# Performance work log

Measured on AMD Instinct MI355X. Metric: run time of the kernel, lower is better.

## Reference

```python
import jax, jax.numpy as jnp
import numpy as np

N, B, T, D = 4, 4, 512, 512
H, DK, DV = 8, 64, 64
LN_EPS = 1e-5


def setup_inputs() -> dict:
    key = jax.random.key(0)
    ks = jax.random.split(key, 5)
    s = 1.0 / np.sqrt(D)
    return {
        "x": jax.random.normal(ks[0], (N, B, T, D), jnp.float32),
        "Wq": jax.random.normal(ks[1], (D, H * DK), jnp.float32) * s,
        "bq": jnp.zeros((H * DK,), jnp.float32),
        "Wk": jax.random.normal(ks[2], (D, H * DK), jnp.float32) * s,
        "bk": jnp.zeros((H * DK,), jnp.float32),
        "Wv": jax.random.normal(ks[3], (D, H * DV), jnp.float32) * s,
        "bv": jnp.zeros((H * DV,), jnp.float32),
        "Wo": jax.random.normal(ks[4], (H * DV, D), jnp.float32) * (1.0 / np.sqrt(H * DV)),
        "bo": jnp.zeros((D,), jnp.float32),
        "gamma": jnp.ones((D,), jnp.float32),
        "beta": jnp.zeros((D,), jnp.float32),
    }


def reference(x, Wq, bq, Wk, bk, Wv, bv, Wo, bo, gamma, beta):
    # x: [N, B, T, D] -- N variables, each [B, T, D]
    n = x.shape[0]
    # Project once per variable (the torch code redundantly recomputes K/V per query var).
    q = (x @ Wq + bq).reshape(n, B, T, H, DK).transpose(0, 1, 3, 2, 4)  # [N,B,H,T,DK]
    k = (x @ Wk + bk).reshape(n, B, T, H, DK).transpose(0, 1, 3, 2, 4)  # [N,B,H,T,DK]
    v = (x @ Wv + bv).reshape(n, B, T, H, DV).transpose(0, 1, 3, 2, 4)  # [N,B,H,T,DV]
    # All-pairs attention: softmax over keys of EACH key-variable separately.
    scores = jnp.einsum('qbhtk,cbhsk->qcbhts', q, k) / np.sqrt(DK)  # [Nq,Nc,B,H,T,T]
    attn = jax.nn.softmax(scores, axis=-1)
    ctx = jnp.einsum('qcbhts,cbhsv->qcbhtv', attn, v)  # [Nq,Nc,B,H,T,DV]
    ctx = ctx.transpose(0, 1, 2, 4, 3, 5).reshape(n, n, B, T, H * DV)
    out = ctx @ Wo + bo                     # per-pair output projection
    out = out.sum(axis=1) / n               # average over key variables -> [N,B,T,D]
    res = x + out
    mu = res.mean(axis=-1, keepdims=True)
    var = res.var(axis=-1, keepdims=True)
    y = (res - mu) / jnp.sqrt(var + LN_EPS) * gamma + beta
    return y
```

## Files before the change

### kernel.cpp

```cpp
#include <hip/hip_runtime.h>


typedef __bf16 bf16x8 __attribute__((ext_vector_type(8)));
typedef __bf16 bf16x4 __attribute__((ext_vector_type(4)));
typedef short shortx4 __attribute__((ext_vector_type(4)));
typedef float floatx4 __attribute__((ext_vector_type(4)));
typedef float floatx16 __attribute__((ext_vector_type(16)));
typedef unsigned short ushortx8 __attribute__((ext_vector_type(8)));

static __device__ __forceinline__ unsigned short f2bf(float f) {
  union { __bf16 h; unsigned short u; } c; c.h = (__bf16)f; return c.u;
}
static __device__ __forceinline__ float bf2f(unsigned short u) {
  union { unsigned u32; float f; } c; c.u32 = ((unsigned)u) << 16; return c.f;
}

#define QSCALE 0.18033688011112042f
#define SHIFT2 (-17.312340489609306f)

__global__ __launch_bounds__(256) void prep(
    const float* __restrict__ Wq, const float* __restrict__ Wk,
    const float* __restrict__ Wv, const float* __restrict__ Wo,
    const float* __restrict__ x,
    unsigned short* __restrict__ wqkvT, unsigned short* __restrict__ woT,
    unsigned short* __restrict__ x_bf)
{
  const int bid = blockIdx.x;
  const int tid = threadIdx.x;
  if (bid < 256) {
    __shared__ unsigned short lds[64][65];
    const int z = bid >> 6, rest = bid & 63;
    const int k0 = (rest >> 3) * 64, n0 = (rest & 7) * 64;
    const float* W; unsigned short* T;
    if (z == 0)      { W = Wq; T = wqkvT; }
    else if (z == 1) { W = Wk; T = wqkvT + 262144; }
    else if (z == 2) { W = Wv; T = wqkvT + 524288; }
    else             { W = Wo; T = woT; }
    const int xx = tid & 63, yy = tid >> 6;
#pragma unroll
    for (int i = 0; i < 16; ++i) {
      const int row = yy * 16 + i;
      lds[row][xx] = f2bf(W[(size_t)(k0 + row) * 512 + n0 + xx]);
    }
    __syncthreads();
#pragma unroll
    for (int i = 0; i < 16; ++i) {
      const int nr = yy * 16 + i;
      T[(size_t)(n0 + nr) * 512 + k0 + xx] = lds[xx][nr];
    }
  } else {
    const int i = (bid - 256) * 256 + tid;
    const float4 a = ((const float4*)x)[i * 2];
    const float4 b = ((const float4*)x)[i * 2 + 1];
    ushortx8 o;
    o[0] = f2bf(a.x); o[1] = f2bf(a.y); o[2] = f2bf(a.z); o[3] = f2bf(a.w);
    o[4] = f2bf(b.x); o[5] = f2bf(b.y); o[6] = f2bf(b.z); o[7] = f2bf(b.w);
    *(ushortx8*)(x_bf + (size_t)i * 8) = o;
  }
}

__global__ __launch_bounds__(256) void gemm_qkv(
    const unsigned short* __restrict__ Xb,
    const unsigned short* __restrict__ BT,
    const float* __restrict__ bq, const float* __restrict__ bk,
    const float* __restrict__ bv,
    unsigned short* __restrict__ Qo, unsigned short* __restrict__ Ko,
    unsigned short* __restrict__ Vo)
{
  __shared__ __align__(16) unsigned short sbuf[18432];
  auto lA = (unsigned short (*)[72])sbuf;
  auto lB = (unsigned short (*)[72])(sbuf + 9216);
  const int tid  = threadIdx.x;
  const int wv   = tid >> 6, lane = tid & 63;
  const int quad = lane >> 4, l16 = lane & 15;
  const int wm = wv >> 1, wn = wv & 1;
  const int m0  = blockIdx.x * 128;
  const int n0g = blockIdx.y * 128;
  const int sel = n0g >> 9;
  const float* bias = (sel == 0) ? bq : (sel == 1) ? bk : bv;
  const float scale = (sel == 0) ? QSCALE : 1.0f;
  unsigned short* outp = (sel == 0) ? Qo : (sel == 1) ? Ko : Vo;

  floatx4 acc[4][4] = {};
  const int srow = tid >> 1, sc0 = (tid & 1) * 32;

  for (int kc = 0; kc < 512; kc += 64) {
    __syncthreads();
    const unsigned short* as = Xb + (size_t)(m0 + srow) * 512 + kc + sc0;
    const unsigned short* bs = BT + (size_t)(n0g + srow) * 512 + kc + sc0;
#pragma unroll
    for (int j = 0; j < 4; ++j) {
      *(bf16x8*)&lA[srow][sc0 + j * 8] = *(const bf16x8*)(as + j * 8);
      *(bf16x8*)&lB[srow][sc0 + j * 8] = *(const bf16x8*)(bs + j * 8);
    }
    __syncthreads();
    bf16x8 af[4][2];
#pragma unroll
    for (int ti = 0; ti < 4; ++ti) {
      af[ti][0] = *(const bf16x8*)&lA[wm * 64 + ti * 16 + l16][quad * 8];
      af[ti][1] = *(const bf16x8*)&lA[wm * 64 + ti * 16 + l16][32 + quad * 8];
    }
#pragma unroll
    for (int ni = 0; ni < 4; ++ni) {
      bf16x8 b0 = *(const bf16x8*)&lB[wn * 64 + ni * 16 + l16][quad * 8];
      bf16x8 b1 = *(const bf16x8*)&lB[wn * 64 + ni * 16 + l16][32 + quad * 8];
#pragma unroll
      for (int ti = 0; ti < 4; ++ti) {
        acc[ti][ni] = __builtin_amdgcn_mfma_f32_16x16x32_bf16(af[ti][0], b0, acc[ti][ni], 0, 0, 0);
        acc[ti][ni] = __builtin_amdgcn_mfma_f32_16x16x32_bf16(af[ti][1], b1, acc[ti][ni], 0, 0, 0);
      }
    }
  }

  if (sel != 2) {
#pragma unroll
    for (int ni = 0; ni < 4; ++ni) {
      const int n = (n0g & 511) + wn * 64 + ni * 16 + l16;
      const float bvv = bias[n];
      const int hh = n >> 6, dk = n & 63;
#pragma unroll
      for (int ti = 0; ti < 4; ++ti) {
        const int mb = m0 + wm * 64 + ti * 16 + quad * 4;
#pragma unroll
        for (int r = 0; r < 4; ++r) {
          const int m = mb + r;
          const int nb = m >> 9, t = m & 511;
          outp[((size_t)(nb * 8 + hh) * 512 + t) * 64 + dk] =
              f2bf((acc[ti][ni][r] + bvv) * scale);
        }
      }
    }
  } else {
    __syncthreads();
    auto tb = (unsigned short (*)[136])sbuf;
#pragma unroll
    for (int ni = 0; ni < 4; ++ni) {
      const int n = (n0g & 511) + wn * 64 + ni * 16 + l16;
      const float bvv = bias[n];
      const int drow = wn * 64 + ni * 16 + l16;
#pragma unroll
      for (int ti = 0; ti < 4; ++ti) {
        const int tcol = wm * 64 + ti * 16 + quad * 4;
        shortx4 pk;
        pk[0] = (short)f2bf(acc[ti][ni][0] + bvv);
        pk[1] = (short)f2bf(acc[ti][ni][1] + bvv);
        pk[2] = (short)f2bf(acc[ti][ni][2] + bvv);
        pk[3] = (short)f2bf(acc[ti][ni][3] + bvv);
        *(shortx4*)&tb[drow][tcol] = pk;
      }
    }
    __syncthreads();
    const int drow = tid >> 1, th = tid & 1;
    const int n = (n0g & 511) + drow;
    const int hh = n >> 6, dk = n & 63;
    const int nb = m0 >> 9, tbase = (m0 & 511) + th * 64;
    unsigned short* gdst = outp + ((size_t)(nb * 8 + hh) * 64 + dk) * 512 + tbase;
#pragma unroll
    for (int j = 0; j < 8; ++j)
      *(ushortx8*)(gdst + j * 8) = *(const ushortx8*)&tb[drow][th * 64 + j * 8];
  }
}

__global__ __launch_bounds__(256) void gemm_out(
    const unsigned short* __restrict__ C0, const unsigned short* __restrict__ C1,
    const unsigned short* __restrict__ BT, unsigned short* __restrict__ Cout)
{
  __shared__ __align__(16) unsigned short lA[128][72];
  __shared__ __align__(16) unsigned short lB[128][72];
  const int tid  = threadIdx.x;
  const int wv   = tid >> 6, lane = tid & 63;
  const int quad = lane >> 4, l16 = lane & 15;
  const int wm = wv >> 1, wn = wv & 1;
  const int m0 = blockIdx.x * 128, n0 = blockIdx.y * 128;

  floatx4 acc[4][4] = {};
  const int srow = tid >> 1, sc0 = (tid & 1) * 32;

  for (int kc = 0; kc < 512; kc += 64) {
    __syncthreads();
    const size_t aoff = (size_t)(m0 + srow) * 512 + kc + sc0;
    const unsigned short* bs = BT + (size_t)(n0 + srow) * 512 + kc + sc0;
#pragma unroll
    for (int j = 0; j < 4; ++j) {
      ushortx8 a0 = *(const ushortx8*)(C0 + aoff + j * 8);
      ushortx8 a1 = *(const ushortx8*)(C1 + aoff + j * 8);
      ushortx8 o;
#pragma unroll
      for (int e = 0; e < 8; ++e) o[e] = f2bf(bf2f(a0[e]) + bf2f(a1[e]));
      *(ushortx8*)&lA[srow][sc0 + j * 8] = o;
      *(bf16x8*)&lB[srow][sc0 + j * 8] = *(const bf16x8*)(bs + j * 8);
    }
    __syncthreads();
    bf16x8 af[4][2];
#pragma unroll
    for (int ti = 0; ti < 4; ++ti) {
      af[ti][0] = *(const bf16x8*)&lA[wm * 64 + ti * 16 + l16][quad * 8];
      af[ti][1] = *(const bf16x8*)&lA[wm * 64 + ti * 16 + l16][32 + quad * 8];
    }
#pragma unroll
    for (int ni = 0; ni < 4; ++ni) {
      bf16x8 b0 = *(const bf16x8*)&lB[wn * 64 + ni * 16 + l16][quad * 8];
      bf16x8 b1 = *(const bf16x8*)&lB[wn * 64 + ni * 16 + l16][32 + quad * 8];
#pragma unroll
      for (int ti = 0; ti < 4; ++ti) {
        acc[ti][ni] = __builtin_amdgcn_mfma_f32_16x16x32_bf16(af[ti][0], b0, acc[ti][ni], 0, 0, 0);
        acc[ti][ni] = __builtin_amdgcn_mfma_f32_16x16x32_bf16(af[ti][1], b1, acc[ti][ni], 0, 0, 0);
      }
    }
  }

#pragma unroll
  for (int ni = 0; ni < 4; ++ni) {
    const int n = n0 + wn * 64 + ni * 16 + l16;
#pragma unroll
    for (int ti = 0; ti < 4; ++ti) {
      const int mb = m0 + wm * 64 + ti * 16 + quad * 4;
#pragma unroll
      for (int r = 0; r < 4; ++r)
        Cout[(size_t)(mb + r) * 512 + n] = f2bf(acc[ti][ni][r]);
    }
  }
}

__global__ __launch_bounds__(256) void flash_kernel(
    const unsigned short* __restrict__ Q,
    const unsigned short* __restrict__ K,
    const unsigned short* __restrict__ VT,
    unsigned short* __restrict__ CTX2)
{
  __shared__ __align__(16) unsigned short lK[2][64][72];
  __shared__ __align__(16) unsigned short lV[2][64][68];
  const int tid  = threadIdx.x;
  const int wv   = tid >> 6, lane = tid & 63;
  const int l32  = lane & 31, u = lane >> 5;

  const int lin  = blockIdx.x;
  const int xcd  = lin & 7, slot = lin >> 3;
  const int tile = slot & 3;
  const int nbh  = xcd * 16 + ((slot >> 2) & 15);
  const int cg   = slot >> 6;
  const int t0   = tile * 128;
  const int h = nbh & 7, nb = nbh >> 3, b = nb & 3;

  const unsigned short* qbase = Q + ((size_t)nbh * 512 + (t0 + wv * 32 + l32)) * 64;
  bf16x8 qf[4];
#pragma unroll
  for (int c16 = 0; c16 < 4; ++c16)
    qf[c16] = *(const bf16x8*)(qbase + c16 * 16 + u * 8);

  const int srow = tid >> 2, sc0 = (tid & 3) * 16;
  const unsigned short *kptr, *vptr;
  auto setptr = [&](int it) {
    const int c = cg * 2 + (it >> 3), s0 = (it & 7) * 64;
    const size_t kvbh = (size_t)((c * 4 + b) * 8 + h);
    kptr = K  + kvbh * (512 * 64) + (size_t)(s0 + srow) * 64 + sc0;
    vptr = VT + kvbh * (64 * 512) + (size_t)srow * 512 + s0 + sc0;
  };
  bf16x8 rk0, rk1, rv0, rv1;
  auto loadregs = [&]() {
    rk0 = *(const bf16x8*)kptr; rk1 = *(const bf16x8*)(kptr + 8);
    rv0 = *(const bf16x8*)vptr; rv1 = *(const bf16x8*)(vptr + 8);
  };
  auto writebuf = [&](int p) {
    *(bf16x8*)&lK[p][srow][sc0]     = rk0;
    *(bf16x8*)&lK[p][srow][sc0 + 8] = rk1;
    union { bf16x8 v8; bf16x4 v4[2]; } c0, c1;
    c0.v8 = rv0; c1.v8 = rv1;
    *(bf16x4*)&lV[p][srow][sc0]      = c0.v4[0];
    *(bf16x4*)&lV[p][srow][sc0 + 4]  = c0.v4[1];
    *(bf16x4*)&lV[p][srow][sc0 + 8]  = c1.v4[0];
    *(bf16x4*)&lV[p][srow][sc0 + 12] = c1.v4[1];
  };

  setptr(0); loadregs();
  writebuf(0);
  setptr(1); loadregs();
  __syncthreads();

  floatx16 ofin0 = {}, ofin1 = {};
  floatx16 oc0, oc1;
  float lacc;

  for (int it = 0; it < 16; ++it) {
    const int cur = it & 1;
    const int st = it & 7;
    if (st == 0) { oc0 = floatx16{}; oc1 = floatx16{}; lacc = 0.f; }

    if (it < 15) writebuf(cur ^ 1);
    if (it < 14) { setptr(it + 2); loadregs(); }

    floatx16 sacc0, sacc1;
#pragma unroll
    for (int r = 0; r < 16; ++r) { sacc0[r] = SHIFT2; sacc1[r] = SHIFT2; }
#pragma unroll
    for (int c16 = 0; c16 < 4; ++c16) {
      bf16x8 ak0 = *(const bf16x8*)&lK[cur][l32][c16 * 16 + u * 8];
      bf16x8 ak1 = *(const bf16x8*)&lK[cur][32 + l32][c16 * 16 + u * 8];
      sacc0 = __builtin_amdgcn_mfma_f32_32x32x16_bf16(ak0, qf[c16], sacc0, 0, 0, 0);
      sacc1 = __builtin_amdgcn_mfma_f32_32x32x16_bf16(ak1, qf[c16], sacc1, 0, 0, 0);
    }

#pragma unroll
    for (int sb = 0; sb < 2; ++sb) {
      const floatx16& sa = sb ? sacc1 : sacc0;
#pragma unroll
      for (int c8 = 0; c8 < 4; ++c8) {
        float e0 = __builtin_amdgcn_exp2f(sa[4 * c8 + 0]);
        float e1 = __builtin_amdgcn_exp2f(sa[4 * c8 + 1]);
        float e2 = __builtin_amdgcn_exp2f(sa[4 * c8 + 2]);
        float e3 = __builtin_amdgcn_exp2f(sa[4 * c8 + 3]);
        lacc += (e0 + e1) + (e2 + e3);
        shortx4 pf;
        pf[0] = (short)f2bf(e0); pf[1] = (short)f2bf(e1);
        pf[2] = (short)f2bf(e2); pf[3] = (short)f2bf(e3);
        const int sloc = sb * 32 + c8 * 8 + u * 4;
        shortx4 vf0 = *(const shortx4*)&lV[cur][l32][sloc];
        shortx4 vf1 = *(const shortx4*)&lV[cur][32 + l32][sloc];
        oc0 = __builtin_amdgcn_mfma_f32_32x32x8bf16_1k(pf, vf0, oc0, 0, 0, 0);
        oc1 = __builtin_amdgcn_mfma_f32_32x32x8bf16_1k(pf, vf1, oc1, 0, 0, 0);
      }
    }

    if (st == 7) {
      float s = lacc;
      s += __shfl_xor(s, 32);
      const float inv = 1.0f / s;
#pragma unroll
      for (int r = 0; r < 16; ++r) {
        const int trow = (r & 3) + 8 * (r >> 2) + 4 * u;
        const float invr = __shfl(inv, trow);
        ofin0[r] += oc0[r] * invr;
        ofin1[r] += oc1[r] * invr;
      }
    }
    __syncthreads();
  }

  unsigned short* outp = CTX2 + (size_t)cg * (8192 * 512);
  const int mbase = nb * 512 + t0 + wv * 32;
#pragma unroll
  for (int r = 0; r < 16; ++r) {
    const int trow = (r & 3) + 8 * (r >> 2) + 4 * u;
    const size_t rowoff = (size_t)(mbase + trow) * 512 + h * 64;
    outp[rowoff + l32]      = f2bf(ofin0[r]);
    outp[rowoff + 32 + l32] = f2bf(ofin1[r]);
  }
}

__global__ __launch_bounds__(256) void ln_kernel(
    const float* __restrict__ x, const unsigned short* __restrict__ tmpb,
    const float* __restrict__ bo, const float* __restrict__ gamma,
    const float* __restrict__ beta, float* __restrict__ out)
{
  const int wv   = threadIdx.x >> 6, lane = threadIdx.x & 63;
  const int row  = blockIdx.x * 4 + wv;
  const int col  = lane * 8;
  const size_t base = (size_t)row * 512 + col;
  const float4 x0 = *(const float4*)(x + base);
  const float4 x1 = *(const float4*)(x + base + 4);
  const ushortx8 t8 = *(const ushortx8*)(tmpb + base);
  const float4 b0 = *(const float4*)(bo + col);
  const float4 b1 = *(const float4*)(bo + col + 4);
  float r[8];
  r[0] = x0.x + 0.25f * bf2f(t8[0]) + b0.x;  r[1] = x0.y + 0.25f * bf2f(t8[1]) + b0.y;
  r[2] = x0.z + 0.25f * bf2f(t8[2]) + b0.z;  r[3] = x0.w + 0.25f * bf2f(t8[3]) + b0.w;
  r[4] = x1.x + 0.25f * bf2f(t8[4]) + b1.x;  r[5] = x1.y + 0.25f * bf2f(t8[5]) + b1.y;
  r[6] = x1.z + 0.25f * bf2f(t8[6]) + b1.z;  r[7] = x1.w + 0.25f * bf2f(t8[7]) + b1.w;
  float s = 0.f, sq = 0.f;
#pragma unroll
  for (int j = 0; j < 8; ++j) { s += r[j]; sq += r[j] * r[j]; }
#pragma unroll
  for (int off = 1; off < 64; off <<= 1) {
    s  += __shfl_xor(s, off);
    sq += __shfl_xor(sq, off);
  }
  const float mu  = s * (1.0f / 512.0f);
  const float var = sq * (1.0f / 512.0f) - mu * mu;
  const float inv = rsqrtf(var + 1e-5f);
  const float4 g0 = *(const float4*)(gamma + col);
  const float4 g1 = *(const float4*)(gamma + col + 4);
  const float4 be0 = *(const float4*)(beta + col);
  const float4 be1 = *(const float4*)(beta + col + 4);
  float4 o0, o1;
  o0.x = (r[0] - mu) * inv * g0.x + be0.x;  o0.y = (r[1] - mu) * inv * g0.y + be0.y;
  o0.z = (r[2] - mu) * inv * g0.z + be0.z;  o0.w = (r[3] - mu) * inv * g0.w + be0.w;
  o1.x = (r[4] - mu) * inv * g1.x + be1.x;  o1.y = (r[5] - mu) * inv * g1.y + be1.y;
  o1.z = (r[6] - mu) * inv * g1.z + be1.z;  o1.w = (r[7] - mu) * inv * g1.w + be1.w;
  *(float4*)(out + base)     = o0;
  *(float4*)(out + base + 4) = o1;
}

extern "C" void kernel_launch(void* const* d_in, const int* in_sizes, int n_in,
                              void* d_out, int out_size, void* d_ws, size_t ws_size,
                              hipStream_t stream) {
  const float* x     = (const float*)d_in[0];
  const float* Wq    = (const float*)d_in[1];
  const float* bq    = (const float*)d_in[2];
  const float* Wk    = (const float*)d_in[3];
  const float* bk    = (const float*)d_in[4];
  const float* Wv    = (const float*)d_in[5];
  const float* bv    = (const float*)d_in[6];
  const float* Wo    = (const float*)d_in[7];
  const float* bo    = (const float*)d_in[8];
  const float* gamma = (const float*)d_in[9];
  const float* beta  = (const float*)d_in[10];
  float* out = (float*)d_out;

  char* w = (char*)d_ws;
  unsigned short* q_bf  = (unsigned short*)(w);
  unsigned short* k_bf  = (unsigned short*)(w + (size_t)8  * 1024 * 1024);
  unsigned short* vt_bf = (unsigned short*)(w + (size_t)16 * 1024 * 1024);
  unsigned short* x_bf  = (unsigned short*)(w + (size_t)24 * 1024 * 1024);
  unsigned short* ctx2  = (unsigned short*)(w + (size_t)24 * 1024 * 1024);
  unsigned short* wqkvT = (unsigned short*)(w + (size_t)40 * 1024 * 1024);
  unsigned short* woT   = wqkvT + 786432;
  unsigned short* tmpb  = (unsigned short*)(w);

  prep<<<2304, 256, 0, stream>>>(Wq, Wk, Wv, Wo, x, wqkvT, woT, x_bf);
  gemm_qkv<<<dim3(64, 12), 256, 0, stream>>>(x_bf, wqkvT, bq, bk, bv,
                                             q_bf, k_bf, vt_bf);
  flash_kernel<<<1024, 256, 0, stream>>>(q_bf, k_bf, vt_bf, ctx2);
  gemm_out<<<dim3(64, 4), 256, 0, stream>>>(ctx2, ctx2 + (size_t)8192 * 512,
                                            woT, tmpb);
  ln_kernel<<<2048, 256, 0, stream>>>(x, tmpb, bo, gamma, beta, out);
}
```

Measured before the change: 195.5 us.

## Fuse x bf16 conversion into QKV GEMM and LayerNorm into output GEMM

Result: slower. 265.5 us (+35.8%).

```diff
diff --git a/kernel.cpp b/kernel.cpp
--- a/kernel.cpp
+++ b/kernel.cpp
@@ -21,46 +21,36 @@
 __global__ __launch_bounds__(256) void prep(
     const float* __restrict__ Wq, const float* __restrict__ Wk,
     const float* __restrict__ Wv, const float* __restrict__ Wo,
-    const float* __restrict__ x,
     unsigned short* __restrict__ wqkvT, unsigned short* __restrict__ woT,
-    unsigned short* __restrict__ x_bf)
+    unsigned int* __restrict__ cnt)
 {
   const int bid = blockIdx.x;
   const int tid = threadIdx.x;
-  if (bid < 256) {
-    __shared__ unsigned short lds[64][65];
-    const int z = bid >> 6, rest = bid & 63;
-    const int k0 = (rest >> 3) * 64, n0 = (rest & 7) * 64;
-    const float* W; unsigned short* T;
-    if (z == 0)      { W = Wq; T = wqkvT; }
-    else if (z == 1) { W = Wk; T = wqkvT + 262144; }
-    else if (z == 2) { W = Wv; T = wqkvT + 524288; }
-    else             { W = Wo; T = woT; }
-    const int xx = tid & 63, yy = tid >> 6;
-#pragma unroll
-    for (int i = 0; i < 16; ++i) {
-      const int row = yy * 16 + i;
-      lds[row][xx] = f2bf(W[(size_t)(k0 + row) * 512 + n0 + xx]);
-    }
-    __syncthreads();
-#pragma unroll
-    for (int i = 0; i < 16; ++i) {
-      const int nr = yy * 16 + i;
-      T[(size_t)(n0 + nr) * 512 + k0 + xx] = lds[xx][nr];
-    }
-  } else {
-    const int i = (bid - 256) * 256 + tid;
-    const float4 a = ((const float4*)x)[i * 2];
-    const float4 b = ((const float4*)x)[i * 2 + 1];
-    ushortx8 o;
-    o[0] = f2bf(a.x); o[1] = f2bf(a.y); o[2] = f2bf(a.z); o[3] = f2bf(a.w);
-    o[4] = f2bf(b.x); o[5] = f2bf(b.y); o[6] = f2bf(b.z); o[7] = f2bf(b.w);
-    *(ushortx8*)(x_bf + (size_t)i * 8) = o;
+  if (bid == 0 && tid < 64) cnt[tid] = 0u;
+  __shared__ unsigned short lds[64][65];
+  const int z = bid >> 6, rest = bid & 63;
+  const int k0 = (rest >> 3) * 64, n0 = (rest & 7) * 64;
+  const float* W; unsigned short* T;
+  if (z == 0)      { W = Wq; T = wqkvT; }
+  else if (z == 1) { W = Wk; T = wqkvT + 262144; }
+  else if (z == 2) { W = Wv; T = wqkvT + 524288; }
+  else             { W = Wo; T = woT; }
+  const int xx = tid & 63, yy = tid >> 6;
+#pragma unroll
+  for (int i = 0; i < 16; ++i) {
+    const int row = yy * 16 + i;
+    lds[row][xx] = f2bf(W[(size_t)(k0 + row) * 512 + n0 + xx]);
+  }
+  __syncthreads();
+#pragma unroll
+  for (int i = 0; i < 16; ++i) {
+    const int nr = yy * 16 + i;
+    T[(size_t)(n0 + nr) * 512 + k0 + xx] = lds[xx][nr];
   }
 }
 
 __global__ __launch_bounds__(256) void gemm_qkv(
-    const unsigned short* __restrict__ Xb,
+    const float* __restrict__ X,
     const unsigned short* __restrict__ BT,
     const float* __restrict__ bq, const float* __restrict__ bk,
     const float* __restrict__ bv,
@@ -86,11 +76,16 @@
 
   for (int kc = 0; kc < 512; kc += 64) {
     __syncthreads();
-    const unsigned short* as = Xb + (size_t)(m0 + srow) * 512 + kc + sc0;
+    const float* as = X + (size_t)(m0 + srow) * 512 + kc + sc0;
     const unsigned short* bs = BT + (size_t)(n0g + srow) * 512 + kc + sc0;
 #pragma unroll
     for (int j = 0; j < 4; ++j) {
-      *(bf16x8*)&lA[srow][sc0 + j * 8] = *(const bf16x8*)(as + j * 8);
+      float4 f0 = *(const float4*)(as + j * 8);
+      float4 f1 = *(const float4*)(as + j * 8 + 4);
+      ushortx8 p;
+      p[0]=f2bf(f0.x); p[1]=f2bf(f0.y); p[2]=f2bf(f0.z); p[3]=f2bf(f0.w);
+      p[4]=f2bf(f1.x); p[5]=f2bf(f1.y); p[6]=f2bf(f1.z); p[7]=f2bf(f1.w);
+      *(ushortx8*)&lA[srow][sc0 + j * 8] = p;
       *(bf16x8*)&lB[srow][sc0 + j * 8] = *(const bf16x8*)(bs + j * 8);
     }
     __syncthreads();
@@ -158,67 +153,6 @@
 #pragma unroll
     for (int j = 0; j < 8; ++j)
       *(ushortx8*)(gdst + j * 8) = *(const ushortx8*)&tb[drow][th * 64 + j * 8];
-  }
-}
-
-__global__ __launch_bounds__(256) void gemm_out(
-    const unsigned short* __restrict__ C0, const unsigned short* __restrict__ C1,
-    const unsigned short* __restrict__ BT, unsigned short* __restrict__ Cout)
-{
-  __shared__ __align__(16) unsigned short lA[128][72];
-  __shared__ __align__(16) unsigned short lB[128][72];
-  const int tid  = threadIdx.x;
-  const int wv   = tid >> 6, lane = tid & 63;
-  const int quad = lane >> 4, l16 = lane & 15;
-  const int wm = wv >> 1, wn = wv & 1;
-  const int m0 = blockIdx.x * 128, n0 = blockIdx.y * 128;
-
-  floatx4 acc[4][4] = {};
-  const int srow = tid >> 1, sc0 = (tid & 1) * 32;
-
-  for (int kc = 0; kc < 512; kc += 64) {
-    __syncthreads();
-    const size_t aoff = (size_t)(m0 + srow) * 512 + kc + sc0;
-    const unsigned short* bs = BT + (size_t)(n0 + srow) * 512 + kc + sc0;
-#pragma unroll
-    for (int j = 0; j < 4; ++j) {
-      ushortx8 a0 = *(const ushortx8*)(C0 + aoff + j * 8);
-      ushortx8 a1 = *(const ushortx8*)(C1 + aoff + j * 8);
-      ushortx8 o;
-#pragma unroll
-      for (int e = 0; e < 8; ++e) o[e] = f2bf(bf2f(a0[e]) + bf2f(a1[e]));
-      *(ushortx8*)&lA[srow][sc0 + j * 8] = o;
-      *(bf16x8*)&lB[srow][sc0 + j * 8] = *(const bf16x8*)(bs + j * 8);
-    }
-    __syncthreads();
-    bf16x8 af[4][2];
-#pragma unroll
-    for (int ti = 0; ti < 4; ++ti) {
-      af[ti][0] = *(const bf16x8*)&lA[wm * 64 + ti * 16 + l16][quad * 8];
-      af[ti][1] = *(const bf16x8*)&lA[wm * 64 + ti * 16 + l16][32 + quad * 8];
-    }
-#pragma unroll
-    for (int ni = 0; ni < 4; ++ni) {
-      bf16x8 b0 = *(const bf16x8*)&lB[wn * 64 + ni * 16 + l16][quad * 8];
-      bf16x8 b1 = *(const bf16x8*)&lB[wn * 64 + ni * 16 + l16][32 + quad * 8];
-#pragma unroll
-      for (int ti = 0; ti < 4; ++ti) {
-        acc[ti][ni] = __builtin_amdgcn_mfma_f32_16x16x32_bf16(af[ti][0], b0, acc[ti][ni], 0, 0, 0);
-        acc[ti][ni] = __builtin_amdgcn_mfma_f32_16x16x32_bf16(af[ti][1], b1, acc[ti][ni], 0, 0, 0);
-      }
-    }
-  }
-
-#pragma unroll
-  for (int ni = 0; ni < 4; ++ni) {
-    const int n = n0 + wn * 64 + ni * 16 + l16;
-#pragma unroll
-    for (int ti = 0; ti < 4; ++ti) {
-      const int mb = m0 + wm * 64 + ti * 16 + quad * 4;
-#pragma unroll
-      for (int r = 0; r < 4; ++r)
-        Cout[(size_t)(mb + r) * 512 + n] = f2bf(acc[ti][ni][r]);
-    }
   }
 }
 
@@ -347,47 +281,113 @@
   }
 }
 
-__global__ __launch_bounds__(256) void ln_kernel(
-    const float* __restrict__ x, const unsigned short* __restrict__ tmpb,
-    const float* __restrict__ bo, const float* __restrict__ gamma,
-    const float* __restrict__ beta, float* __restrict__ out)
+__global__ __launch_bounds__(256) void gemm_out_ln(
+    const unsigned short* __restrict__ C0, const unsigned short* __restrict__ C1,
+    const unsigned short* __restrict__ BT, unsigned short* __restrict__ tmpb,
+    const float* __restrict__ x, const float* __restrict__ bo,
+    const float* __restrict__ gamma, const float* __restrict__ beta,
+    float* __restrict__ out, unsigned int* __restrict__ cnt)
 {
-  const int wv   = threadIdx.x >> 6, lane = threadIdx.x & 63;
-  const int row  = blockIdx.x * 4 + wv;
-  const int col  = lane * 8;
-  const size_t base = (size_t)row * 512 + col;
-  const float4 x0 = *(const float4*)(x + base);
-  const float4 x1 = *(const float4*)(x + base + 4);
-  const ushortx8 t8 = *(const ushortx8*)(tmpb + base);
-  const float4 b0 = *(const float4*)(bo + col);
-  const float4 b1 = *(const float4*)(bo + col + 4);
-  float r[8];
-  r[0] = x0.x + 0.25f * bf2f(t8[0]) + b0.x;  r[1] = x0.y + 0.25f * bf2f(t8[1]) + b0.y;
-  r[2] = x0.z + 0.25f * bf2f(t8[2]) + b0.z;  r[3] = x0.w + 0.25f * bf2f(t8[3]) + b0.w;
-  r[4] = x1.x + 0.25f * bf2f(t8[4]) + b1.x;  r[5] = x1.y + 0.25f * bf2f(t8[5]) + b1.y;
-  r[6] = x1.z + 0.25f * bf2f(t8[6]) + b1.z;  r[7] = x1.w + 0.25f * bf2f(t8[7]) + b1.w;
-  float s = 0.f, sq = 0.f;
-#pragma unroll
-  for (int j = 0; j < 8; ++j) { s += r[j]; sq += r[j] * r[j]; }
-#pragma unroll
-  for (int off = 1; off < 64; off <<= 1) {
-    s  += __shfl_xor(s, off);
-    sq += __shfl_xor(sq, off);
-  }
-  const float mu  = s * (1.0f / 512.0f);
-  const float var = sq * (1.0f / 512.0f) - mu * mu;
-  const float inv = rsqrtf(var + 1e-5f);
-  const float4 g0 = *(const float4*)(gamma + col);
-  const float4 g1 = *(const float4*)(gamma + col + 4);
-  const float4 be0 = *(const float4*)(beta + col);
-  const float4 be1 = *(const float4*)(beta + col + 4);
-  float4 o0, o1;
-  o0.x = (r[0] - mu) * inv * g0.x + be0.x;  o0.y = (r[1] - mu) * inv * g0.y + be0.y;
-  o0.z = (r[2] - mu) * inv * g0.z + be0.z;  o0.w = (r[3] - mu) * inv * g0.w + be0.w;
-  o1.x = (r[4] - mu) * inv * g1.x + be1.x;  o1.y = (r[5] - mu) * inv * g1.y + be1.y;
-  o1.z = (r[6] - mu) * inv * g1.z + be1.z;  o1.w = (r[7] - mu) * inv * g1.w + be1.w;
-  *(float4*)(out + base)     = o0;
-  *(float4*)(out + base + 4) = o1;
+  __shared__ __align__(16) unsigned short lA[128][72];
+  __shared__ __align__(16) unsigned short lB[128][72];
+  const int tid  = threadIdx.x;
+  const int wv   = tid >> 6, lane = tid & 63;
+  const int quad = lane >> 4, l16 = lane & 15;
+  const int wm = wv >> 1, wn = wv & 1;
+  const int m0 = blockIdx.x * 128, n0 = blockIdx.y * 128;
+
+  floatx4 acc[4][4] = {};
+  const int srow = tid >> 1, sc0 = (tid & 1) * 32;
+
+  for (int kc = 0; kc < 512; kc += 64) {
+    __syncthreads();
+    const size_t aoff = (size_t)(m0 + srow) * 512 + kc + sc0;
+    const unsigned short* bs = BT + (size_t)(n0 + srow) * 512 + kc + sc0;
+#pragma unroll
+    for (int j = 0; j < 4; ++j) {
+      ushortx8 a0 = *(const ushortx8*)(C0 + aoff + j * 8);
+      ushortx8 a1 = *(const ushortx8*)(C1 + aoff + j * 8);
+      ushortx8 o;
+#pragma unroll
+      for (int e = 0; e < 8; ++e) o[e] = f2bf(bf2f(a0[e]) + bf2f(a1[e]));
+      *(ushortx8*)&lA[srow][sc0 + j * 8] = o;
+      *(bf16x8*)&lB[srow][sc0 + j * 8] = *(const bf16x8*)(bs + j * 8);
+    }
+    __syncthreads();
+    bf16x8 af[4][2];
+#pragma unroll
+    for (int ti = 0; ti < 4; ++ti) {
+      af[ti][0] = *(const bf16x8*)&lA[wm * 64 + ti * 16 + l16][quad * 8];
+      af[ti][1] = *(const bf16x8*)&lA[wm * 64 + ti * 16 + l16][32 + quad * 8];
+    }
+#pragma unroll
+    for (int ni = 0; ni < 4; ++ni) {
+      bf16x8 b0 = *(const bf16x8*)&lB[wn * 64 + ni * 16 + l16][quad * 8];
+      bf16x8 b1 = *(const bf16x8*)&lB[wn * 64 + ni * 16 + l16][32 + quad * 8];
+#pragma unroll
+      for (int ti = 0; ti < 4; ++ti) {
+        acc[ti][ni] = __builtin_amdgcn_mfma_f32_16x16x32_bf16(af[ti][0], b0, acc[ti][ni], 0, 0, 0);
+        acc[ti][ni] = __builtin_amdgcn_mfma_f32_16x16x32_bf16(af[ti][1], b1, acc[ti][ni], 0, 0, 0);
+      }
+    }
+  }
+
+#pragma unroll
+  for (int ni = 0; ni < 4; ++ni) {
+    const int n = n0 + wn * 64 + ni * 16 + l16;
+#pragma unroll
+    for (int ti = 0; ti < 4; ++ti) {
+      const int mb = m0 + wm * 64 + ti * 16 + quad * 4;
+#pragma unroll
+      for (int r = 0; r < 4; ++r)
+        tmpb[(size_t)(mb + r) * 512 + n] = f2bf(acc[ti][ni][r]);
+    }
+  }
+
+  __threadfence();
+  __shared__ unsigned int lastdone;
+  if (tid == 0) lastdone = (atomicAdd(&cnt[blockIdx.x], 1u) == 3u) ? 1u : 0u;
+  __syncthreads();
+  if (lastdone) {
+    __threadfence();
+    const int col = lane * 8;
+    const float4 b0 = *(const float4*)(bo + col);
+    const float4 b1 = *(const float4*)(bo + col + 4);
+    const float4 g0 = *(const float4*)(gamma + col);
+    const float4 g1 = *(const float4*)(gamma + col + 4);
+    const float4 be0 = *(const float4*)(beta + col);
+    const float4 be1 = *(const float4*)(beta + col + 4);
+    for (int rr = 0; rr < 32; ++rr) {
+      const int row = m0 + wv * 32 + rr;
+      const size_t base = (size_t)row * 512 + col;
+      const float4 x0 = *(const float4*)(x + base);
+      const float4 x1 = *(const float4*)(x + base + 4);
+      const ushortx8 t8 = *(const ushortx8*)(tmpb + base);
+      float r[8];
+      r[0] = x0.x + 0.25f * bf2f(t8[0]) + b0.x;  r[1] = x0.y + 0.25f * bf2f(t8[1]) + b0.y;
+      r[2] = x0.z + 0.25f * bf2f(t8[2]) + b0.z;  r[3] = x0.w + 0.25f * bf2f(t8[3]) + b0.w;
+      r[4] = x1.x + 0.25f * bf2f(t8[4]) + b1.x;  r[5] = x1.y + 0.25f * bf2f(t8[5]) + b1.y;
+      r[6] = x1.z + 0.25f * bf2f(t8[6]) + b1.z;  r[7] = x1.w + 0.25f * bf2f(t8[7]) + b1.w;
+      float s = 0.f, sq = 0.f;
+#pragma unroll
+      for (int j = 0; j < 8; ++j) { s += r[j]; sq += r[j] * r[j]; }
+#pragma unroll
+      for (int off = 1; off < 64; off <<= 1) {
+        s  += __shfl_xor(s, off);
+        sq += __shfl_xor(sq, off);
+      }
+      const float mu  = s * (1.0f / 512.0f);
+      const float var = sq * (1.0f / 512.0f) - mu * mu;
+      const float inv = rsqrtf(var + 1e-5f);
+      float4 o0, o1;
+      o0.x = (r[0] - mu) * inv * g0.x + be0.x;  o0.y = (r[1] - mu) * inv * g0.y + be0.y;
+      o0.z = (r[2] - mu) * inv * g0.z + be0.z;  o0.w = (r[3] - mu) * inv * g0.w + be0.w;
+      o1.x = (r[4] - mu) * inv * g1.x + be1.x;  o1.y = (r[5] - mu) * inv * g1.y + be1.y;
+      o1.z = (r[6] - mu) * inv * g1.z + be1.z;  o1.w = (r[7] - mu) * inv * g1.w + be1.w;
+      *(float4*)(out + base)     = o0;
+      *(float4*)(out + base + 4) = o1;
+    }
+  }
 }
 
 extern "C" void kernel_launch(void* const* d_in, const int* in_sizes, int n_in,
@@ -410,17 +410,17 @@
   unsigned short* q_bf  = (unsigned short*)(w);
   unsigned short* k_bf  = (unsigned short*)(w + (size_t)8  * 1024 * 1024);
   unsigned short* vt_bf = (unsigned short*)(w + (size_t)16 * 1024 * 1024);
-  unsigned short* x_bf  = (unsigned short*)(w + (size_t)24 * 1024 * 1024);
   unsigned short* ctx2  = (unsigned short*)(w + (size_t)24 * 1024 * 1024);
-  unsigned short* wqkvT = (unsigned short*)(w + (size_t)40 * 1024 * 1024);
+  unsigned int*   cnt   = (unsigned int*)(w + (size_t)40 * 1024 * 1024);
+  unsigned short* wqkvT = (unsigned short*)(w + (size_t)40 * 1024 * 1024 + 1024);
   unsigned short* woT   = wqkvT + 786432;
   unsigned short* tmpb  = (unsigned short*)(w);
 
-  prep<<<2304, 256, 0, stream>>>(Wq, Wk, Wv, Wo, x, wqkvT, woT, x_bf);
-  gemm_qkv<<<dim3(64, 12), 256, 0, stream>>>(x_bf, wqkvT, bq, bk, bv,
+  prep<<<256, 256, 0, stream>>>(Wq, Wk, Wv, Wo, wqkvT, woT, cnt);
+  gemm_qkv<<<dim3(64, 12), 256, 0, stream>>>(x, wqkvT, bq, bk, bv,
                                              q_bf, k_bf, vt_bf);
   flash_kernel<<<1024, 256, 0, stream>>>(q_bf, k_bf, vt_bf, ctx2);
-  gemm_out<<<dim3(64, 4), 256, 0, stream>>>(ctx2, ctx2 + (size_t)8192 * 512,
-                                            woT, tmpb);
-  ln_kernel<<<2048, 256, 0, stream>>>(x, tmpb, bo, gamma, beta, out);
-}
+  gemm_out_ln<<<dim3(64, 4), 256, 0, stream>>>(ctx2, ctx2 + (size_t)8192 * 512,
+                                               woT, tmpb, x, bo, gamma, beta,
+                                               out, cnt);
+}
```
